# Kernel tuning notes

Hardware: AMD Instinct MI355X
Metric: run time of the kernel (lower is better)

Reference implementation:

```python
import jax, jax.numpy as jnp
import numpy as np

H = 1024
R = 16


def setup_inputs() -> dict:
    key = jax.random.key(0)
    ks = jax.random.split(key, 9)
    s = 1.0 / np.sqrt(H)
    x = jax.random.normal(ks[0], (8192, H), dtype=jnp.float32)
    # gate (rule_attention): Linear(H, R)
    Wa = jax.random.uniform(ks[1], (H, R), minval=-s, maxval=s, dtype=jnp.float32)
    ba = jax.random.uniform(ks[2], (R,), minval=-s, maxval=s, dtype=jnp.float32)
    # stacked rule_heads: R x (Linear(H,H) -> ReLU -> Linear(H,H))
    W1 = jax.random.uniform(ks[3], (R, H, H), minval=-s, maxval=s, dtype=jnp.float32)
    b1 = jax.random.uniform(ks[4], (R, H), minval=-s, maxval=s, dtype=jnp.float32)
    W2 = jax.random.uniform(ks[5], (R, H, H), minval=-s, maxval=s, dtype=jnp.float32)
    b2 = jax.random.uniform(ks[6], (R, H), minval=-s, maxval=s, dtype=jnp.float32)
    # stacked rule_confidence: R x (Linear(H,1) -> Sigmoid)
    Wc = jax.random.uniform(ks[7], (R, H), minval=-s, maxval=s, dtype=jnp.float32)
    bc = jax.random.uniform(ks[8], (R,), minval=-s, maxval=s, dtype=jnp.float32)
    return {"x": x, "Wa": Wa, "ba": ba, "W1": W1, "b1": b1,
            "W2": W2, "b2": b2, "Wc": Wc, "bc": bc}


def reference(x, Wa, ba, W1, b1, W2, b2, Wc, bc):
    # gate: softmax over rules               [B, R]
    attention = jax.nn.softmax(x @ Wa + ba, axis=-1)
    # all rule MLPs as one batched matmul    [B, R, H]
    h = jax.nn.relu(jnp.einsum("bh,rhd->brd", x, W1) + b1)
    outputs = jnp.einsum("brd,rdo->bro", h, W2) + b2
    # per-rule confidence                    [B, R]
    confidences = jax.nn.sigmoid(jnp.einsum("bh,rh->br", x, Wc) + bc)
    # combine gate with confidence, renormalize, weighted sum over rules
    combined = attention * confidences
    combined = combined / (combined.sum(axis=-1, keepdims=True) + 1e-8)
    output = jnp.einsum("bro,br->bo", outputs, combined)  # [B, H]
    return output, confidences
```

## Files before the change

kernel.cpp:

```cpp
#include <hip/hip_runtime.h>

typedef __attribute__((ext_vector_type(8))) short short8;
typedef __attribute__((ext_vector_type(4))) float f32x4;

#define B_SZ 8192
#define H_SZ 1024
#define R_SZ 16

__device__ __forceinline__ unsigned short f2bf(float f) {
  union { float f; unsigned u; } v; v.f = f;
  unsigned u = v.u + 0x7FFFu + ((v.u >> 16) & 1u);
  return (unsigned short)(u >> 16);
}

__global__ __launch_bounds__(256) void transpose_cvt(const float* __restrict__ src,
                                                     unsigned short* __restrict__ dst,
                                                     int rows, int cols) {
  __shared__ float t[32][33];
  size_t zoff = (size_t)blockIdx.z * (size_t)rows * cols;
  int c0 = blockIdx.x * 32, r0 = blockIdx.y * 32;
  int tx = threadIdx.x, ty = threadIdx.y;
#pragma unroll
  for (int i = 0; i < 4; ++i)
    t[ty + 8 * i][tx] = src[zoff + (size_t)(r0 + ty + 8 * i) * cols + c0 + tx];
  __syncthreads();
#pragma unroll
  for (int i = 0; i < 4; ++i)
    dst[zoff + (size_t)(c0 + ty + 8 * i) * rows + r0 + tx] = f2bf(t[tx][ty + 8 * i]);
}

__global__ __launch_bounds__(256) void transpose_wa(const float* __restrict__ Wa,
                                                    float* __restrict__ WaT) {
  int t = blockIdx.x * 256 + threadIdx.x;
  int h = t >> 4, r = t & 15;
  WaT[r * H_SZ + h] = Wa[t];
}

__global__ __launch_bounds__(256) void gate_kernel(const float* __restrict__ x,
                                                   const float* __restrict__ WaT,
                                                   const float* __restrict__ ba,
                                                   const float* __restrict__ Wc,
                                                   const float* __restrict__ bc,
                                                   float* __restrict__ comb,
                                                   float* __restrict__ conf,
                                                   unsigned short* __restrict__ xb) {
  int b = blockIdx.x * 4 + (threadIdx.x >> 6);
  int l = threadIdx.x & 63;
  const float* xr = x + (size_t)b * H_SZ;
  unsigned short* xbr = xb + (size_t)b * H_SZ;
  float xv[16];
#pragma unroll
  for (int j = 0; j < 16; ++j) xv[j] = xr[l + 64 * j];
#pragma unroll
  for (int j = 0; j < 16; ++j) xbr[l + 64 * j] = f2bf(xv[j]);
  float la[16], lcf[16];
#pragma unroll
  for (int r = 0; r < 16; ++r) {
    float sa = 0.f, sc = 0.f;
#pragma unroll
    for (int j = 0; j < 16; ++j) {
      int h = l + 64 * j;
      sa += xv[j] * WaT[r * H_SZ + h];
      sc += xv[j] * Wc[r * H_SZ + h];
    }
#pragma unroll
    for (int off = 32; off > 0; off >>= 1) {
      sa += __shfl_xor(sa, off);
      sc += __shfl_xor(sc, off);
    }
    la[r] = sa + ba[r];
    lcf[r] = sc + bc[r];
  }
  float mx = la[0];
#pragma unroll
  for (int r = 1; r < 16; ++r) mx = fmaxf(mx, la[r]);
  float se = 0.f;
#pragma unroll
  for (int r = 0; r < 16; ++r) { la[r] = expf(la[r] - mx); se += la[r]; }
  float cb[16]; float cs = 0.f;
#pragma unroll
  for (int r = 0; r < 16; ++r) {
    float cf = 1.f / (1.f + expf(-lcf[r]));
    lcf[r] = cf;
    cb[r] = (la[r] / se) * cf;
    cs += cb[r];
  }
  float inv = 1.f / (cs + 1e-8f);
  if (l < 16) {
    float cv = 0.f, qv = 0.f;
#pragma unroll
    for (int r = 0; r < 16; ++r)
      if (r == l) { cv = lcf[r]; qv = cb[r] * inv; }
    conf[b * 16 + l] = cv;
    comb[b * 16 + l] = qv;
  }
}

template <int MODE>
__global__ __launch_bounds__(256) void gemm_nt(
    const unsigned short* __restrict__ A, int lda,
    const unsigned short* __restrict__ B, int ldb, int K,
    unsigned short* __restrict__ Hp, int ldh,
    const float* __restrict__ b1v,
    float* __restrict__ Out,
    const float* __restrict__ b2v,
    const float* __restrict__ comb,
    int r_base, int accum) {
  __shared__ short smem[16384];
  short* As = smem;
  short* Bs = smem + 8192;

  const int tid = threadIdx.x;
  const int lane = tid & 63;
  const int wid = tid >> 6;
  const int wm = wid >> 1, wn = wid & 1;
  const int lr = lane >> 4, lc = lane & 15;

  const int bn0 = blockIdx.x * 128;
  const int bm0 = blockIdx.y * 128;

  int srow[4], ssc[4];
#pragma unroll
  for (int i = 0; i < 4; ++i) {
    int idx = i * 256 + tid;
    srow[i] = idx >> 3;
    ssc[i] = idx & 7;
  }

  const f32x4 zero = {0.f, 0.f, 0.f, 0.f};
  f32x4 acc[4][4];
#pragma unroll
  for (int i = 0; i < 4; ++i)
#pragma unroll
    for (int j = 0; j < 4; ++j) acc[i][j] = zero;

  const int KT = K >> 6;

  short8 va[4], vb[4];
#pragma unroll
  for (int i = 0; i < 4; ++i) {
    va[i] = *(const short8*)(A + (size_t)(bm0 + srow[i]) * lda + ssc[i] * 8);
    vb[i] = *(const short8*)(B + (size_t)(bn0 + srow[i]) * ldb + ssc[i] * 8);
  }

  for (int kt = 0; kt < KT; ++kt) {
    __syncthreads();
#pragma unroll
    for (int i = 0; i < 4; ++i) {
      *(short8*)(As + srow[i] * 64 + ((ssc[i] ^ (srow[i] & 7)) * 8)) = va[i];
      *(short8*)(Bs + srow[i] * 64 + ((ssc[i] ^ (srow[i] & 7)) * 8)) = vb[i];
    }
    __syncthreads();
    if (kt + 1 < KT) {
      int k0 = (kt + 1) << 6;
#pragma unroll
      for (int i = 0; i < 4; ++i) {
        va[i] = *(const short8*)(A + (size_t)(bm0 + srow[i]) * lda + k0 + ssc[i] * 8);
        vb[i] = *(const short8*)(B + (size_t)(bn0 + srow[i]) * ldb + k0 + ssc[i] * 8);
      }
    }
#pragma unroll
    for (int c = 0; c < 2; ++c) {
      short8 af[4], bfr[4];
#pragma unroll
      for (int f = 0; f < 4; ++f) {
        int ra = wm * 64 + f * 16 + lc;
        af[f] = *(const short8*)(As + ra * 64 + (((c * 4 + lr) ^ (ra & 7)) * 8));
        int rb = wn * 64 + f * 16 + lc;
        bfr[f] = *(const short8*)(Bs + rb * 64 + (((c * 4 + lr) ^ (rb & 7)) * 8));
      }
#pragma unroll
      for (int mf = 0; mf < 4; ++mf)
#pragma unroll
        for (int nf = 0; nf < 4; ++nf)
          acc[mf][nf] = __builtin_amdgcn_mfma_f32_16x16x32_bf16(af[mf], bfr[nf],
                                                                acc[mf][nf], 0, 0, 0);
    }
  }

#pragma unroll
  for (int mf = 0; mf < 4; ++mf) {
#pragma unroll
    for (int nf = 0; nf < 4; ++nf) {
      int m0 = bm0 + wm * 64 + mf * 16 + lr * 4;
      int n = bn0 + wn * 64 + nf * 16 + lc;
      f32x4 a = acc[mf][nf];
      if (MODE == 0) {
        int r = r_base + (n >> 10);
        int d = n & 1023;
        float bias = b1v[r * H_SZ + d];
#pragma unroll
        for (int j = 0; j < 4; ++j) {
          float v = fmaxf(a[j] + bias, 0.f) * comb[(size_t)(m0 + j) * 16 + r];
          Hp[(size_t)(m0 + j) * ldh + n] = f2bf(v);
        }
      } else {
#pragma unroll
        for (int j = 0; j < 4; ++j) {
          size_t row = (size_t)(m0 + j);
          float v = a[j];
          if (accum) {
            v += Out[row * H_SZ + n];
          } else {
            float bs = 0.f;
#pragma unroll
            for (int r = 0; r < 16; ++r)
              bs += comb[row * 16 + r] * b2v[r * H_SZ + n];
            v += bs;
          }
          Out[row * H_SZ + n] = v;
        }
      }
    }
  }
}

extern "C" void kernel_launch(void* const* d_in, const int* in_sizes, int n_in,
                              void* d_out, int out_size, void* d_ws, size_t ws_size,
                              hipStream_t stream) {
  if (n_in < 9) return;
  const float* x  = (const float*)d_in[0];
  const float* Wa = (const float*)d_in[1];
  const float* ba = (const float*)d_in[2];
  const float* W1 = (const float*)d_in[3];
  const float* b1 = (const float*)d_in[4];
  const float* W2 = (const float*)d_in[5];
  const float* b2 = (const float*)d_in[6];
  const float* Wc = (const float*)d_in[7];
  const float* bc = (const float*)d_in[8];

  float* out = (float*)d_out;
  float* conf = out + (size_t)B_SZ * H_SZ;

  char* w = (char*)d_ws;
  unsigned short* xb = (unsigned short*)w;  w += (size_t)B_SZ * H_SZ * 2;
  unsigned short* W1T = (unsigned short*)w; w += (size_t)R_SZ * H_SZ * H_SZ * 2;
  unsigned short* W2T = (unsigned short*)w; w += (size_t)R_SZ * H_SZ * H_SZ * 2;
  float* comb = (float*)w;                  w += (size_t)B_SZ * R_SZ * 4;
  float* WaT = (float*)w;                   w += (size_t)R_SZ * H_SZ * 4;
  unsigned short* Hp = (unsigned short*)w;
  size_t used = (size_t)(w - (char*)d_ws);

  int G = 16;
  while (G > 1 && used + (size_t)B_SZ * G * H_SZ * 2 > ws_size) G >>= 1;
  if (used + (size_t)B_SZ * G * H_SZ * 2 > ws_size) return;

  dim3 tb(32, 8);
  transpose_cvt<<<dim3(32, 32, 16), tb, 0, stream>>>(W1, W1T, H_SZ, H_SZ);
  transpose_cvt<<<dim3(32, 512, 1), tb, 0, stream>>>(W2, W2T, R_SZ * H_SZ, H_SZ);
  transpose_wa<<<dim3(64), dim3(256), 0, stream>>>(Wa, WaT);
  gate_kernel<<<dim3(B_SZ / 4), dim3(256), 0, stream>>>(x, WaT, ba, Wc, bc, comb, conf, xb);

  int ngroups = R_SZ / G;
  for (int g = 0; g < ngroups; ++g) {
    gemm_nt<0><<<dim3(G * 8, 64), dim3(256), 0, stream>>>(
        xb, H_SZ,
        W1T + (size_t)g * G * H_SZ * H_SZ, H_SZ, H_SZ,
        Hp, G * H_SZ, b1, nullptr, nullptr, comb, g * G, 0);
    gemm_nt<1><<<dim3(8, 64), dim3(256), 0, stream>>>(
        Hp, G * H_SZ,
        W2T + (size_t)g * G * H_SZ, R_SZ * H_SZ, G * H_SZ,
        nullptr, 0, nullptr, out, b2, comb, 0, (g > 0) ? 1 : 0);
  }
}
```

Baseline: 758.8 us.

## Replace GEMM with 256-row tiles, async global-to-LDS loads and 8-phase pipelining

Replaces the 128x128, 256-thread GEMM with 512-thread blocks covering 256-row tiles (256 or 128 columns). Tiles go straight from global memory into double-buffered LDS via global_load_lds, and each k-step is split into eight phases that interleave staging with MFMA issue under raised wave priority. The aim is more operand reuse per block and hidden global latency in both rule-MLP GEMMs. The cost is much more LDS and register pressure (one block per CU), and on the second GEMM only 256 blocks, which may underfill the device.

```diff
diff --git a/kernel.cpp b/kernel.cpp
--- a/kernel.cpp
+++ b/kernel.cpp
@@ -96,95 +96,123 @@
   }
 }
 
-template <int MODE>
-__global__ __launch_bounds__(256) void gemm_nt(
+__device__ __forceinline__ void gload16(const unsigned short* g, const unsigned short* l) {
+  __builtin_amdgcn_global_load_lds(
+      (const __attribute__((address_space(1))) unsigned int*)g,
+      (__attribute__((address_space(3))) unsigned int*)(unsigned short*)l, 16, 0, 0);
+}
+
+#define VMCNT0 asm volatile("s_waitcnt vmcnt(0)" ::: "memory")
+#define NOP ((void)0)
+
+template <int BN, int MODE>
+__global__ __launch_bounds__(512, 1) void gemm8p(
     const unsigned short* __restrict__ A, int lda,
-    const unsigned short* __restrict__ B, int ldb, int K,
+    const unsigned short* __restrict__ Bm, int ldb, int K,
     unsigned short* __restrict__ Hp, int ldh,
     const float* __restrict__ b1v,
     float* __restrict__ Out,
     const float* __restrict__ b2v,
     const float* __restrict__ comb,
     int r_base, int accum) {
-  __shared__ short smem[16384];
-  short* As = smem;
-  short* Bs = smem + 8192;
+  constexpr int ASZ = 256 * 64;
+  constexpr int BSZ = BN * 64;
+  constexpr int NQ = BN / 128;
+  constexpr int BLOADS = BN / 64;
+  __shared__ unsigned short smem[2 * (ASZ + BSZ)];
 
   const int tid = threadIdx.x;
   const int lane = tid & 63;
   const int wid = tid >> 6;
-  const int wm = wid >> 1, wn = wid & 1;
+  const int wm = wid >> 2;
+  const int wn = wid & 3;
   const int lr = lane >> 4, lc = lane & 15;
-
-  const int bn0 = blockIdx.x * 128;
-  const int bm0 = blockIdx.y * 128;
-
-  int srow[4], ssc[4];
-#pragma unroll
-  for (int i = 0; i < 4; ++i) {
-    int idx = i * 256 + tid;
-    srow[i] = idx >> 3;
-    ssc[i] = idx & 7;
-  }
-
-  const f32x4 zero = {0.f, 0.f, 0.f, 0.f};
-  f32x4 acc[4][4];
-#pragma unroll
-  for (int i = 0; i < 4; ++i)
-#pragma unroll
-    for (int j = 0; j < 4; ++j) acc[i][j] = zero;
-
+  const int bn0 = blockIdx.x * BN;
+  const int bm0 = blockIdx.y * 256;
   const int KT = K >> 6;
 
-  short8 va[4], vb[4];
-#pragma unroll
-  for (int i = 0; i < 4; ++i) {
-    va[i] = *(const short8*)(A + (size_t)(bm0 + srow[i]) * lda + ssc[i] * 8);
-    vb[i] = *(const short8*)(B + (size_t)(bn0 + srow[i]) * ldb + ssc[i] * 8);
-  }
-
-  for (int kt = 0; kt < KT; ++kt) {
-    __syncthreads();
-#pragma unroll
-    for (int i = 0; i < 4; ++i) {
-      *(short8*)(As + srow[i] * 64 + ((ssc[i] ^ (srow[i] & 7)) * 8)) = va[i];
-      *(short8*)(Bs + srow[i] * 64 + ((ssc[i] ^ (srow[i] & 7)) * 8)) = vb[i];
-    }
-    __syncthreads();
-    if (kt + 1 < KT) {
-      int k0 = (kt + 1) << 6;
-#pragma unroll
-      for (int i = 0; i < 4; ++i) {
-        va[i] = *(const short8*)(A + (size_t)(bm0 + srow[i]) * lda + k0 + ssc[i] * 8);
-        vb[i] = *(const short8*)(B + (size_t)(bn0 + srow[i]) * ldb + k0 + ssc[i] * 8);
-      }
-    }
-#pragma unroll
-    for (int c = 0; c < 2; ++c) {
-      short8 af[4], bfr[4];
-#pragma unroll
-      for (int f = 0; f < 4; ++f) {
-        int ra = wm * 64 + f * 16 + lc;
-        af[f] = *(const short8*)(As + ra * 64 + (((c * 4 + lr) ^ (ra & 7)) * 8));
-        int rb = wn * 64 + f * 16 + lc;
-        bfr[f] = *(const short8*)(Bs + rb * 64 + (((c * 4 + lr) ^ (rb & 7)) * 8));
-      }
-#pragma unroll
-      for (int mf = 0; mf < 4; ++mf)
-#pragma unroll
-        for (int nf = 0; nf < 4; ++nf)
-          acc[mf][nf] = __builtin_amdgcn_mfma_f32_16x16x32_bf16(af[mf], bfr[nf],
-                                                                acc[mf][nf], 0, 0, 0);
-    }
-  }
-
-#pragma unroll
-  for (int mf = 0; mf < 4; ++mf) {
-#pragma unroll
-    for (int nf = 0; nf < 4; ++nf) {
-      int m0 = bm0 + wm * 64 + mf * 16 + lr * 4;
-      int n = bn0 + wn * 64 + nf * 16 + lc;
-      f32x4 a = acc[mf][nf];
+  f32x4 acc[8][2 * NQ];
+#pragma unroll
+  for (int i = 0; i < 8; ++i)
+#pragma unroll
+    for (int j = 0; j < 2 * NQ; ++j) acc[i][j] = {0.f, 0.f, 0.f, 0.f};
+
+  auto stageA = [&](int bf, int kt) {
+    const unsigned short* base = smem + (bf ? (ASZ + BSZ) : 0);
+#pragma unroll
+    for (int q = 0; q < 4; ++q) {
+      int rl = (q * 512 + tid) >> 3;
+      int ck = (tid & 7) ^ (rl & 7);
+      gload16(A + (size_t)(bm0 + rl) * lda + kt * 64 + ck * 8,
+              base + q * 4096 + (tid & ~63) * 8);
+    }
+  };
+  auto stageB = [&](int bf, int kt) {
+    const unsigned short* base = smem + (bf ? (ASZ + BSZ) : 0) + ASZ;
+#pragma unroll
+    for (int q = 0; q < BLOADS; ++q) {
+      int rl = (q * 512 + tid) >> 3;
+      int ck = (tid & 7) ^ (rl & 7);
+      gload16(Bm + (size_t)(bn0 + rl) * ldb + kt * 64 + ck * 8,
+              base + q * 4096 + (tid & ~63) * 8);
+    }
+  };
+
+#define PHASE(BF, MH, NH, STG, TAIL)                                               \
+  {                                                                                \
+    const unsigned short* As = smem + (BF ? (ASZ + BSZ) : 0);                      \
+    const unsigned short* Bs = As + ASZ;                                           \
+    short8 af[2][4];                                                               \
+    short8 bg[2][NQ];                                                              \
+    _Pragma("unroll") for (int c = 0; c < 2; ++c) {                                \
+      _Pragma("unroll") for (int f = 0; f < 4; ++f) {                              \
+        int ra = wm * 128 + MH * 64 + f * 16 + lc;                                 \
+        af[c][f] = *(const short8*)(As + ra * 64 + (((c * 4 + lr) ^ (ra & 7)) * 8)); \
+      }                                                                            \
+      _Pragma("unroll") for (int g = 0; g < NQ; ++g) {                             \
+        int rb = wn * (BN / 4) + NH * (BN / 8) + g * 16 + lc;                      \
+        bg[c][g] = *(const short8*)(Bs + rb * 64 + (((c * 4 + lr) ^ (rb & 7)) * 8)); \
+      }                                                                            \
+    }                                                                              \
+    STG;                                                                           \
+    __builtin_amdgcn_s_barrier();                                                  \
+    __builtin_amdgcn_s_setprio(1);                                                 \
+    _Pragma("unroll") for (int c = 0; c < 2; ++c)                                  \
+      _Pragma("unroll") for (int f = 0; f < 4; ++f)                                \
+        _Pragma("unroll") for (int g = 0; g < NQ; ++g)                             \
+          acc[MH * 4 + f][NH * NQ + g] = __builtin_amdgcn_mfma_f32_16x16x32_bf16(  \
+              af[c][f], bg[c][g], acc[MH * 4 + f][NH * NQ + g], 0, 0, 0);          \
+    __builtin_amdgcn_s_setprio(0);                                                 \
+    TAIL;                                                                          \
+    __builtin_amdgcn_s_barrier();                                                  \
+  }
+
+  stageA(0, 0);
+  stageB(0, 0);
+  VMCNT0;
+  __builtin_amdgcn_s_barrier();
+
+  const int P = KT >> 1;
+  for (int i = 0; i < P; ++i) {
+    const int t1 = 2 * i + 1, t2 = 2 * i + 2;
+    PHASE(0, 0, 0, stageA(1, t1), NOP)
+    PHASE(0, 0, 1, stageB(1, t1), NOP)
+    PHASE(0, 1, 0, NOP, NOP)
+    PHASE(0, 1, 1, NOP, VMCNT0)
+    PHASE(1, 0, 0, if (t2 < KT) stageA(0, t2), NOP)
+    PHASE(1, 0, 1, if (t2 < KT) stageB(0, t2), NOP)
+    PHASE(1, 1, 0, NOP, NOP)
+    PHASE(1, 1, 1, NOP, VMCNT0)
+  }
+#undef PHASE
+
+#pragma unroll
+  for (int ii = 0; ii < 8; ++ii) {
+#pragma unroll
+    for (int jj = 0; jj < 2 * NQ; ++jj) {
+      int m0 = bm0 + wm * 128 + ii * 16 + lr * 4;
+      int n = bn0 + wn * (BN / 4) + jj * 16 + lc;
+      f32x4 a = acc[ii][jj];
       if (MODE == 0) {
         int r = r_base + (n >> 10);
         int d = n & 1023;
@@ -253,11 +281,11 @@
 
   int ngroups = R_SZ / G;
   for (int g = 0; g < ngroups; ++g) {
-    gemm_nt<0><<<dim3(G * 8, 64), dim3(256), 0, stream>>>(
+    gemm8p<256, 0><<<dim3(G * 4, B_SZ / 256), dim3(512), 0, stream>>>(
         xb, H_SZ,
         W1T + (size_t)g * G * H_SZ * H_SZ, H_SZ, H_SZ,
         Hp, G * H_SZ, b1, nullptr, nullptr, comb, g * G, 0);
-    gemm_nt<1><<<dim3(8, 64), dim3(256), 0, stream>>>(
+    gemm8p<128, 1><<<dim3(H_SZ / 128, B_SZ / 256), dim3(512), 0, stream>>>(
         Hp, G * H_SZ,
         W2T + (size_t)g * G * H_SZ, R_SZ * H_SZ, G * H_SZ,
         nullptr, 0, nullptr, out, b2, comb, 0, (g > 0) ? 1 : 0);
```

Result: slower. 877.8 us (+15.7%).

## Rewrite GEMM with direct-to-LDS loads, triple buffering, and 256x128 tiles

Applied to the files above, without the earlier changes.

Replaces the register-staged double-buffered GEMM with a kernel that loads tiles straight into LDS through global_load_lds, keeps a three-stage buffer ring and waits with explicit vmcnt counters. It also raises the block to 512 threads covering 256x128 output tiles, and it raises wave priority around the MFMA bursts. The goal is to overlap global loads with matrix math and cut register pressure and VGPR-to-LDS copies. In exchange the kernel uses much more LDS, which limits it to one block per CU, and the hand-placed waitcnt and barrier logic is fragile.

```diff
diff --git a/kernel.cpp b/kernel.cpp
--- a/kernel.cpp
+++ b/kernel.cpp
@@ -96,95 +96,117 @@
   }
 }
 
+__device__ __forceinline__ void gload16(const unsigned short* g, const unsigned short* l) {
+  __builtin_amdgcn_global_load_lds(
+      (const __attribute__((address_space(1))) unsigned int*)g,
+      (__attribute__((address_space(3))) unsigned int*)(unsigned short*)l, 16, 0, 0);
+}
+
 template <int MODE>
-__global__ __launch_bounds__(256) void gemm_nt(
+__global__ __launch_bounds__(512, 1) void gemm3b(
     const unsigned short* __restrict__ A, int lda,
-    const unsigned short* __restrict__ B, int ldb, int K,
+    const unsigned short* __restrict__ Bm, int ldb, int K,
     unsigned short* __restrict__ Hp, int ldh,
     const float* __restrict__ b1v,
     float* __restrict__ Out,
     const float* __restrict__ b2v,
     const float* __restrict__ comb,
     int r_base, int accum) {
-  __shared__ short smem[16384];
-  short* As = smem;
-  short* Bs = smem + 8192;
+  constexpr int ABUF = 256 * 64;
+  constexpr int BBUF = 128 * 64;
+  constexpr int BUFE = ABUF + BBUF;
+  __shared__ unsigned short smem[3 * BUFE];
 
   const int tid = threadIdx.x;
   const int lane = tid & 63;
   const int wid = tid >> 6;
-  const int wm = wid >> 1, wn = wid & 1;
+  const int wm = wid >> 1;
+  const int wn = wid & 1;
   const int lr = lane >> 4, lc = lane & 15;
-
   const int bn0 = blockIdx.x * 128;
-  const int bm0 = blockIdx.y * 128;
-
-  int srow[4], ssc[4];
-#pragma unroll
-  for (int i = 0; i < 4; ++i) {
-    int idx = i * 256 + tid;
-    srow[i] = idx >> 3;
-    ssc[i] = idx & 7;
-  }
-
-  const f32x4 zero = {0.f, 0.f, 0.f, 0.f};
+  const int bm0 = blockIdx.y * 256;
+  const int KT = K >> 6;
+
   f32x4 acc[4][4];
 #pragma unroll
   for (int i = 0; i < 4; ++i)
 #pragma unroll
-    for (int j = 0; j < 4; ++j) acc[i][j] = zero;
-
-  const int KT = K >> 6;
-
-  short8 va[4], vb[4];
-#pragma unroll
-  for (int i = 0; i < 4; ++i) {
-    va[i] = *(const short8*)(A + (size_t)(bm0 + srow[i]) * lda + ssc[i] * 8);
-    vb[i] = *(const short8*)(B + (size_t)(bn0 + srow[i]) * ldb + ssc[i] * 8);
-  }
-
-  for (int kt = 0; kt < KT; ++kt) {
-    __syncthreads();
-#pragma unroll
-    for (int i = 0; i < 4; ++i) {
-      *(short8*)(As + srow[i] * 64 + ((ssc[i] ^ (srow[i] & 7)) * 8)) = va[i];
-      *(short8*)(Bs + srow[i] * 64 + ((ssc[i] ^ (srow[i] & 7)) * 8)) = vb[i];
-    }
-    __syncthreads();
-    if (kt + 1 < KT) {
-      int k0 = (kt + 1) << 6;
-#pragma unroll
-      for (int i = 0; i < 4; ++i) {
-        va[i] = *(const short8*)(A + (size_t)(bm0 + srow[i]) * lda + k0 + ssc[i] * 8);
-        vb[i] = *(const short8*)(B + (size_t)(bn0 + srow[i]) * ldb + k0 + ssc[i] * 8);
-      }
-    }
-#pragma unroll
-    for (int c = 0; c < 2; ++c) {
-      short8 af[4], bfr[4];
-#pragma unroll
-      for (int f = 0; f < 4; ++f) {
-        int ra = wm * 64 + f * 16 + lc;
-        af[f] = *(const short8*)(As + ra * 64 + (((c * 4 + lr) ^ (ra & 7)) * 8));
-        int rb = wn * 64 + f * 16 + lc;
-        bfr[f] = *(const short8*)(Bs + rb * 64 + (((c * 4 + lr) ^ (rb & 7)) * 8));
-      }
-#pragma unroll
-      for (int mf = 0; mf < 4; ++mf)
-#pragma unroll
-        for (int nf = 0; nf < 4; ++nf)
-          acc[mf][nf] = __builtin_amdgcn_mfma_f32_16x16x32_bf16(af[mf], bfr[nf],
-                                                                acc[mf][nf], 0, 0, 0);
-    }
-  }
-
-#pragma unroll
-  for (int mf = 0; mf < 4; ++mf) {
-#pragma unroll
-    for (int nf = 0; nf < 4; ++nf) {
-      int m0 = bm0 + wm * 64 + mf * 16 + lr * 4;
-      int n = bn0 + wn * 64 + nf * 16 + lc;
-      f32x4 a = acc[mf][nf];
+    for (int j = 0; j < 4; ++j) acc[i][j] = {0.f, 0.f, 0.f, 0.f};
+
+  auto stage = [&](int buf, int kt) {
+    const unsigned short* base = smem + buf * BUFE;
+#pragma unroll
+    for (int q = 0; q < 4; ++q) {
+      int rl = (q * 512 + tid) >> 3;
+      int ck = (tid & 7) ^ (rl & 7);
+      gload16(A + (size_t)(bm0 + rl) * lda + kt * 64 + ck * 8,
+              base + q * 4096 + (tid & ~63) * 8);
+    }
+#pragma unroll
+    for (int q = 0; q < 2; ++q) {
+      int rl = (q * 512 + tid) >> 3;
+      int ck = (tid & 7) ^ (rl & 7);
+      gload16(Bm + (size_t)(bn0 + rl) * ldb + kt * 64 + ck * 8,
+              base + ABUF + q * 4096 + (tid & ~63) * 8);
+    }
+  };
+
+  stage(0, 0);
+  stage(1, 1);
+  asm volatile("s_waitcnt vmcnt(6)" ::: "memory");
+  __builtin_amdgcn_s_barrier();
+
+  for (int t = 0; t < KT; ++t) {
+    const unsigned short* As = smem + (t % 3) * BUFE;
+    const unsigned short* Bs = As + ABUF;
+    short8 af[4], bg[4];
+#pragma unroll
+    for (int f = 0; f < 4; ++f) {
+      int ra = wm * 64 + f * 16 + lc;
+      af[f] = *(const short8*)(As + ra * 64 + ((lr ^ (ra & 7)) * 8));
+      int rb = wn * 64 + f * 16 + lc;
+      bg[f] = *(const short8*)(Bs + rb * 64 + ((lr ^ (rb & 7)) * 8));
+    }
+    if (t + 2 < KT) stage((t + 2) % 3, t + 2);
+    __builtin_amdgcn_s_barrier();
+    __builtin_amdgcn_s_setprio(1);
+#pragma unroll
+    for (int f = 0; f < 4; ++f)
+#pragma unroll
+      for (int g = 0; g < 4; ++g)
+        acc[f][g] = __builtin_amdgcn_mfma_f32_16x16x32_bf16(af[f], bg[g], acc[f][g], 0, 0, 0);
+    __builtin_amdgcn_s_setprio(0);
+    __builtin_amdgcn_s_barrier();
+#pragma unroll
+    for (int f = 0; f < 4; ++f) {
+      int ra = wm * 64 + f * 16 + lc;
+      af[f] = *(const short8*)(As + ra * 64 + (((4 + lr) ^ (ra & 7)) * 8));
+      int rb = wn * 64 + f * 16 + lc;
+      bg[f] = *(const short8*)(Bs + rb * 64 + (((4 + lr) ^ (rb & 7)) * 8));
+    }
+    __builtin_amdgcn_s_barrier();
+    __builtin_amdgcn_s_setprio(1);
+#pragma unroll
+    for (int f = 0; f < 4; ++f)
+#pragma unroll
+      for (int g = 0; g < 4; ++g)
+        acc[f][g] = __builtin_amdgcn_mfma_f32_16x16x32_bf16(af[f], bg[g], acc[f][g], 0, 0, 0);
+    __builtin_amdgcn_s_setprio(0);
+    if (t + 2 < KT) {
+      asm volatile("s_waitcnt vmcnt(6)" ::: "memory");
+    } else if (t + 1 < KT) {
+      asm volatile("s_waitcnt vmcnt(0)" ::: "memory");
+    }
+    __builtin_amdgcn_s_barrier();
+  }
+
+#pragma unroll
+  for (int f = 0; f < 4; ++f) {
+#pragma unroll
+    for (int g = 0; g < 4; ++g) {
+      int m0 = bm0 + wm * 64 + f * 16 + lr * 4;
+      int n = bn0 + wn * 64 + g * 16 + lc;
+      f32x4 a = acc[f][g];
       if (MODE == 0) {
         int r = r_base + (n >> 10);
         int d = n & 1023;
@@ -253,11 +275,11 @@
 
   int ngroups = R_SZ / G;
   for (int g = 0; g < ngroups; ++g) {
-    gemm_nt<0><<<dim3(G * 8, 64), dim3(256), 0, stream>>>(
+    gemm3b<0><<<dim3(G * 8, B_SZ / 256), dim3(512), 0, stream>>>(
         xb, H_SZ,
         W1T + (size_t)g * G * H_SZ * H_SZ, H_SZ, H_SZ,
         Hp, G * H_SZ, b1, nullptr, nullptr, comb, g * G, 0);
-    gemm_nt<1><<<dim3(8, 64), dim3(256), 0, stream>>>(
+    gemm3b<1><<<dim3(H_SZ / 128, B_SZ / 256), dim3(512), 0, stream>>>(
         Hp, G * H_SZ,
         W2T + (size_t)g * G * H_SZ, R_SZ * H_SZ, G * H_SZ,
         nullptr, 0, nullptr, out, b2, comb, 0, (g > 0) ? 1 : 0);
```

After: 792.9 us. 4.5% more time.

## Add 256x256 eight-wave pipelined GEMM for the first rule-MLP layer

Applied to the files above, without the earlier changes.

Adds a new 512-thread bf16 MFMA GEMM kernel with 256x256 tiles. It stages data with global_load_lds direct-to-LDS loads into XOR-swizzled double buffers, and interleaves partial LDS reads, async prefetches and MFMA quarters under barriers and setprio. The kernel replaces the 128x128 gemm_nt for the W1 layer, which is the larger GEMM (B x 16H x H), to raise data reuse and overlap memory with compute. It needs large LDS (128KB) and one block per CU, and depends on the barrier/vmcnt choreography being correct. The second GEMM launch is unchanged apart from rewriting its grid with named constants.

```diff
diff --git a/kernel.cpp b/kernel.cpp
--- a/kernel.cpp
+++ b/kernel.cpp
@@ -96,6 +96,167 @@
   }
 }
 
+__device__ __forceinline__ void gload16(const unsigned short* g, const unsigned short* l) {
+  __builtin_amdgcn_global_load_lds(
+      (const __attribute__((address_space(1))) unsigned int*)g,
+      (__attribute__((address_space(3))) unsigned int*)(unsigned short*)l, 16, 0, 0);
+}
+
+#define RDA(DST, MH)                                                                   \
+  _Pragma("unroll") for (int c = 0; c < 2; ++c)                                        \
+  _Pragma("unroll") for (int f = 0; f < 4; ++f) {                                      \
+    int ra = (MH) * 128 + wm * 64 + f * 16 + lc;                                       \
+    DST[c][f] = *(const short8*)(bufp + ra * 64 + (((c * 4 + lr) ^ (ra & 7)) * 8));    \
+  }
+#define RDB(DST, NH)                                                                   \
+  _Pragma("unroll") for (int c = 0; c < 2; ++c)                                        \
+  _Pragma("unroll") for (int g = 0; g < 2; ++g) {                                      \
+    int rb = (NH) * 128 + wn * 32 + g * 16 + lc;                                       \
+    DST[c][g] = *(const short8*)(bufp + ABM + rb * 64 + (((c * 4 + lr) ^ (rb & 7)) * 8)); \
+  }
+#define MF(AS, BS, MH, NH)                                                             \
+  __builtin_amdgcn_s_setprio(1);                                                       \
+  _Pragma("unroll") for (int c = 0; c < 2; ++c)                                        \
+  _Pragma("unroll") for (int f = 0; f < 4; ++f)                                        \
+  _Pragma("unroll") for (int g = 0; g < 2; ++g)                                        \
+    acc[(MH) * 4 + f][(NH) * 2 + g] = __builtin_amdgcn_mfma_f32_16x16x32_bf16(         \
+        AS[c][f], BS[c][g], acc[(MH) * 4 + f][(NH) * 2 + g], 0, 0, 0);                 \
+  __builtin_amdgcn_s_setprio(0);
+#define LGKM0                                                                          \
+  asm volatile("s_waitcnt lgkmcnt(0)" ::: "memory");                                   \
+  __builtin_amdgcn_sched_barrier(0);
+
+template <int MODE>
+__global__ __launch_bounds__(512, 1) void gemm8f(
+    const unsigned short* __restrict__ A, int lda,
+    const unsigned short* __restrict__ Bm, int ldb, int K,
+    unsigned short* __restrict__ Hp, int ldh,
+    const float* __restrict__ b1v,
+    float* __restrict__ Out,
+    const float* __restrict__ b2v,
+    const float* __restrict__ comb,
+    int r_base, int accum) {
+  constexpr int ABM = 256 * 64;
+  constexpr int BUFE = 2 * ABM;
+  __shared__ unsigned short smem[2 * BUFE];
+
+  const int tid = threadIdx.x;
+  const int lane = tid & 63;
+  const int wid = tid >> 6;
+  const int wm = wid >> 2, wn = wid & 3;
+  const int lr = lane >> 4, lc = lane & 15;
+  const int bn0 = blockIdx.x * 256;
+  const int bm0 = blockIdx.y * 256;
+  const int KT = K >> 6;
+
+  f32x4 acc[8][4];
+#pragma unroll
+  for (int i = 0; i < 8; ++i)
+#pragma unroll
+    for (int j = 0; j < 4; ++j) acc[i][j] = {0.f, 0.f, 0.f, 0.f};
+
+  auto stageA = [&](int buf, int kt, int h) {
+#pragma unroll
+    for (int q = 0; q < 2; ++q) {
+      int idx = q * 512 + tid;
+      int row = h * 128 + (idx >> 3);
+      int ck = (idx & 7) ^ (row & 7);
+      gload16(A + (size_t)(bm0 + row) * lda + kt * 64 + ck * 8,
+              smem + buf * BUFE + h * 8192 + (q * 512 + (tid & ~63)) * 8);
+    }
+  };
+  auto stageB = [&](int buf, int kt, int h) {
+#pragma unroll
+    for (int q = 0; q < 2; ++q) {
+      int idx = q * 512 + tid;
+      int row = h * 128 + (idx >> 3);
+      int ck = (idx & 7) ^ (row & 7);
+      gload16(Bm + (size_t)(bn0 + row) * ldb + kt * 64 + ck * 8,
+              smem + buf * BUFE + ABM + h * 8192 + (q * 512 + (tid & ~63)) * 8);
+    }
+  };
+
+  stageA(0, 0, 0); stageB(0, 0, 0); stageB(0, 0, 1); stageA(0, 0, 1);
+  stageA(1, 1, 0); stageB(1, 1, 0); stageB(1, 1, 1);
+  asm volatile("s_waitcnt vmcnt(6)" ::: "memory");
+  __builtin_amdgcn_s_barrier();
+
+  for (int t = 0; t < KT; ++t) {
+    const unsigned short* bufp = smem + (t & 1) * BUFE;
+    const int nb = (t & 1) ^ 1;
+    const int cb = (t & 1);
+    short8 a0[2][4], a1[2][4], b0[2][2], b1h[2][2];
+
+    RDA(a0, 0)
+    RDB(b0, 0)
+    if (t + 1 < KT) stageA(nb, t + 1, 1);
+    __builtin_amdgcn_s_barrier();
+    LGKM0
+    MF(a0, b0, 0, 0)
+    __builtin_amdgcn_s_barrier();
+
+    RDB(b1h, 1)
+    if (t + 2 < KT) stageA(cb, t + 2, 0);
+    __builtin_amdgcn_s_barrier();
+    LGKM0
+    MF(a0, b1h, 0, 1)
+    __builtin_amdgcn_s_barrier();
+
+    RDA(a1, 1)
+    if (t + 2 < KT) stageB(cb, t + 2, 0);
+    __builtin_amdgcn_s_barrier();
+    LGKM0
+    MF(a1, b1h, 1, 1)
+    __builtin_amdgcn_s_barrier();
+
+    if (t + 2 < KT) stageB(cb, t + 2, 1);
+    __builtin_amdgcn_s_barrier();
+    MF(a1, b0, 1, 0)
+    asm volatile("s_waitcnt vmcnt(6)" ::: "memory");
+    __builtin_amdgcn_s_barrier();
+  }
+
+#pragma unroll
+  for (int i = 0; i < 8; ++i) {
+#pragma unroll
+    for (int j = 0; j < 4; ++j) {
+      int m0 = bm0 + (i >> 2) * 128 + wm * 64 + (i & 3) * 16 + lr * 4;
+      int n = bn0 + (j >> 1) * 128 + wn * 32 + (j & 1) * 16 + lc;
+      f32x4 a = acc[i][j];
+      if (MODE == 0) {
+        int r = r_base + (n >> 10);
+        int d = n & 1023;
+        float bias = b1v[r * H_SZ + d];
+#pragma unroll
+        for (int jj = 0; jj < 4; ++jj) {
+          float v = fmaxf(a[jj] + bias, 0.f) * comb[(size_t)(m0 + jj) * 16 + r];
+          Hp[(size_t)(m0 + jj) * ldh + n] = f2bf(v);
+        }
+      } else {
+#pragma unroll
+        for (int jj = 0; jj < 4; ++jj) {
+          size_t row = (size_t)(m0 + jj);
+          float v = a[jj];
+          if (accum) {
+            v += Out[row * H_SZ + n];
+          } else {
+            float bs = 0.f;
+#pragma unroll
+            for (int r = 0; r < 16; ++r)
+              bs += comb[row * 16 + r] * b2v[r * H_SZ + n];
+            v += bs;
+          }
+          Out[row * H_SZ + n] = v;
+        }
+      }
+    }
+  }
+}
+#undef RDA
+#undef RDB
+#undef MF
+#undef LGKM0
+
 template <int MODE>
 __global__ __launch_bounds__(256) void gemm_nt(
     const unsigned short* __restrict__ A, int lda,
@@ -253,11 +414,11 @@
 
   int ngroups = R_SZ / G;
   for (int g = 0; g < ngroups; ++g) {
-    gemm_nt<0><<<dim3(G * 8, 64), dim3(256), 0, stream>>>(
+    gemm8f<0><<<dim3(G * H_SZ / 256, B_SZ / 256), dim3(512), 0, stream>>>(
         xb, H_SZ,
         W1T + (size_t)g * G * H_SZ * H_SZ, H_SZ, H_SZ,
         Hp, G * H_SZ, b1, nullptr, nullptr, comb, g * G, 0);
-    gemm_nt<1><<<dim3(8, 64), dim3(256), 0, stream>>>(
+    gemm_nt<1><<<dim3(H_SZ / 128, B_SZ / 128), dim3(256), 0, stream>>>(
         Hp, G * H_SZ,
         W2T + (size_t)g * G * H_SZ, R_SZ * H_SZ, G * H_SZ,
         nullptr, 0, nullptr, out, b2, comb, 0, (g > 0) ? 1 : 0);
```

Result: faster. 728.7 us (median of 2 runs) (-4.0%).
